# Optimization experiments

Hardware: AMD Instinct MI355X
Metric: run time of the kernel (lower is better)

The kernel has to match this reference:

```python
import jax, jax.numpy as jnp
import numpy as np

NUM_HEADS = 8

def conv1x1(w, x, b=None):
    # w: [O, C], x: [B, C, H, W] -> [B, O, H, W]
    y = jnp.einsum('oc,bchw->bohw', w, x)
    if b is not None:
        y = y + b[None, :, None, None]
    return y

def setup_inputs() -> dict:
    key = jax.random.key(0)
    ks = jax.random.split(key, 8)
    B, C, H, W = 8, 512, 32, 32
    s = lambda fan: 1.0 / np.sqrt(fan)
    return {
        'x': jax.random.normal(ks[0], (B, C, H, W), jnp.float32),
        'W_qkv': jax.random.normal(ks[1], (3 * C, C), jnp.float32) * s(C),
        'W_proj': jax.random.normal(ks[2], (C, C), jnp.float32) * s(C),
        'b_proj': jax.random.normal(ks[3], (C,), jnp.float32) * 0.01,
        'W_att1': jax.random.normal(ks[4], (C // 4, C), jnp.float32) * s(C),
        'b_att1': jax.random.normal(ks[5], (C // 4,), jnp.float32) * 0.01,
        'W_att2': jax.random.normal(ks[6], (1, C // 4), jnp.float32) * s(C // 4),
        'b_att2': jax.random.normal(ks[7], (1,), jnp.float32) * 0.01,
    }

def reference(x, W_qkv, W_proj, b_proj, W_att1, b_att1, W_att2, b_att2):
    B, C, H, W = x.shape
    nh = NUM_HEADS
    dh = C // nh
    N = H * W
    qkv = conv1x1(W_qkv, x)                      # [B, 3C, H, W]
    qkv = qkv.reshape(B, 3, nh, dh, N)
    qkv = jnp.transpose(qkv, (1, 0, 2, 4, 3))    # [3, B, nh, N, dh]
    q, k, v = qkv[0], qkv[1], qkv[2]
    attn = jnp.einsum('bhnd,bhmd->bhnm', q, k) * (dh ** -0.5)
    attn = jax.nn.softmax(attn, axis=-1)         # dropout is identity at eval
    o = jnp.einsum('bhnm,bhmd->bhnd', attn, v)   # [B, nh, N, dh]
    # Faithful to torch: transpose(1,2) then raw reshape to (B, C, H, W)
    o = jnp.swapaxes(o, 1, 2).reshape(B, C, H, W)
    out = conv1x1(W_proj, o, b_proj)             # [B, C, H, W]
    h1 = jax.nn.relu(conv1x1(W_att1, out, b_att1))
    spatial_att = jax.nn.sigmoid(conv1x1(W_att2, h1, b_att2))  # [B, 1, H, W]
    out = out * spatial_att
    return (out, spatial_att)
```

## Files before the change

kernel.cpp:

```cpp
#include <hip/hip_runtime.h>
#include <hip/hip_bf16.h>

using bf16 = __hip_bfloat16;
typedef __bf16 bf16x8 __attribute__((ext_vector_type(8)));
typedef float  f32x4  __attribute__((ext_vector_type(4)));


static constexpr int B  = 8;
static constexpr int C  = 512;
static constexpr int N  = 1024;
static constexpr int NH = 8;
static constexpr int DH = 64;
static constexpr int CQ = 128;

static constexpr float QSCALE = 0.125f * 1.44269504f;

static constexpr size_t QKV_OFF  = 0;
static constexpr size_t H1_OFF   = 25165824;

__device__ __forceinline__ unsigned pack2(float lo, float hi) {
  __hip_bfloat162 h = __float22bfloat162_rn(make_float2(lo, hi));
  return *(unsigned*)&h;
}
__device__ __forceinline__ int swz(int row, int col) {
  return row * 64 + ((((col >> 3) ^ row) & 7) << 3) + (col & 7);
}
__device__ __forceinline__ bf16x8 ldfrag(const short* tl, int row, int kk, int lane) {
  const int atom = 4 * kk + (lane >> 4);
  return *(const bf16x8*)&tl[row * 64 + (((atom ^ row) & 7) << 3)];
}
__device__ __forceinline__ bf16x8 ldfragF(const short* tl, int row, int kk, int lane) {
  const int atom = 4 * kk + (lane >> 4);
  return *(const bf16x8*)&tl[row * 64 + (((atom ^ row ^ (row >> 2)) & 7) << 3)];
}
__device__ __forceinline__ int fswz(int row, int col) {
  return row * 64 + ((((col >> 2) ^ row) & 15) << 2) + (col & 3);
}
__device__ __forceinline__ void swap32(unsigned &a, unsigned &b) {
  asm("v_permlane32_swap_b32 %0, %1" : "+v"(a), "+v"(b));
}
__device__ __forceinline__ void swap16(unsigned &a, unsigned &b) {
  asm("v_permlane16_swap_b32 %0, %1" : "+v"(a), "+v"(b));
}

__global__ __launch_bounds__(256, 3) void k_qkv(const float* __restrict__ W,
                                                const float* __restrict__ x,
                                                bf16* __restrict__ qkv) {
  __shared__ __align__(16) short Al[128 * 64];
  __shared__ __align__(16) short Bl[128 * 64];
  const int pt = blockIdx.x, ot = blockIdx.y, b = blockIdx.z;
  const int p0 = pt * 128, o0 = ot * 128;
  const int t = threadIdx.x, l = t & 63, w = t >> 6;
  const int wo = w & 1, wp = w >> 1;
  const int g = t >> 5, k32 = t & 31;
  const int r16 = t >> 4, q16 = t & 15;
  const float* xsrc = x + ((size_t)b * C + 8 * g) * N + p0 + 4 * k32;
  const float* wsrc = W + (size_t)(o0 + r16) * C + 4 * q16;
  unsigned upx[16], upw[16];
  auto ld = [&](int kc) {
    const float* xa = xsrc + (size_t)kc * N;
#pragma unroll
    for (int u = 0; u < 4; ++u) {
      float4 r0 = *(const float4*)(xa + (size_t)(2 * u) * N);
      float4 r1 = *(const float4*)(xa + (size_t)(2 * u + 1) * N);
      upx[4*u+0] = pack2(r0.x, r1.x);
      upx[4*u+1] = pack2(r0.y, r1.y);
      upx[4*u+2] = pack2(r0.z, r1.z);
      upx[4*u+3] = pack2(r0.w, r1.w);
    }
    const float* wa = wsrc + kc;
#pragma unroll
    for (int i = 0; i < 8; ++i) {
      float4 f = *(const float4*)(wa + (size_t)(16 * i) * C);
      upw[2*i]   = pack2(f.x, f.y);
      upw[2*i+1] = pack2(f.z, f.w);
    }
  };
  f32x4 acc[4][4] = {};
  ld(0);
  for (int kc = 0; kc < C; kc += 64) {
    __syncthreads();
#pragma unroll
    for (int j = 0; j < 4; ++j) {
      const int p = 4 * k32 + j;
      uint4 v = make_uint4(upx[j], upx[4 + j], upx[8 + j], upx[12 + j]);
      *(uint4*)&Al[p * 64 + (((g ^ p ^ (p >> 2)) & 7) << 3)] = v;
    }
#pragma unroll
    for (int i = 0; i < 8; ++i) {
      const int R = 16 * i + r16;
      *(uint2*)&Bl[R * 64 + ((((q16 >> 1) ^ R) & 7) << 3) + 4 * (q16 & 1)] =
          make_uint2(upw[2 * i], upw[2 * i + 1]);
    }
    __syncthreads();
    if (kc + 64 < C) ld(kc + 64);
#pragma unroll
    for (int kk = 0; kk < 2; ++kk) {
      bf16x8 af[4], bf[4];
#pragma unroll
      for (int i = 0; i < 4; ++i) af[i] = ldfrag(Bl, wo*64 + i*16 + (l&15), kk, l);
#pragma unroll
      for (int j = 0; j < 4; ++j) bf[j] = ldfragF(Al, wp*64 + j*16 + (l&15), kk, l);
#pragma unroll
      for (int i = 0; i < 4; ++i)
#pragma unroll
        for (int j = 0; j < 4; ++j)
          acc[i][j] = __builtin_amdgcn_mfma_f32_16x16x32_bf16(af[i], bf[j], acc[i][j], 0, 0, 0);
    }
  }
  const float qs = (ot < 4) ? QSCALE : 1.0f;
  __syncthreads();
  {
    short* T = wo ? Bl : Al;
#pragma unroll
    for (int i = 0; i < 4; ++i) {
      const int d = i * 16 + 4 * (l >> 4);
#pragma unroll
      for (int j = 0; j < 4; ++j) {
        const int p = wp * 64 + j * 16 + (l & 15);
        *(unsigned*)&T[swz(p, d)]     = pack2(acc[i][j][0] * qs, acc[i][j][1] * qs);
        *(unsigned*)&T[swz(p, d + 2)] = pack2(acc[i][j][2] * qs, acc[i][j][3] * qs);
      }
    }
  }
  __syncthreads();
  {
    const int oc0 = o0, oc1 = o0 + 64;
    bf16* dst0 = qkv + (size_t)(oc0 >> 9) * (B * NH * N * DH) +
                 (size_t)(b * NH + ((oc0 >> 6) & 7)) * N * DH + (size_t)p0 * DH;
    bf16* dst1 = qkv + (size_t)(oc1 >> 9) * (B * NH * N * DH) +
                 (size_t)(b * NH + ((oc1 >> 6) & 7)) * N * DH + (size_t)p0 * DH;
#pragma unroll
    for (int it = 0; it < 8; ++it) {
      const int e = t + 256 * it;
      const int tile = e >> 10, row = (e >> 3) & 127, atom = e & 7;
      const short* T = tile ? Bl : Al;
      uint4 val = *(const uint4*)&T[row * 64 + (((atom ^ row) & 7) << 3)];
      bf16* dst = tile ? dst1 : dst0;
      *(uint4*)(dst + (size_t)row * DH + atom * 8) = val;
    }
  }
}

__global__ __launch_bounds__(256) void k_attn(bf16* __restrict__ qkv) {
  __shared__ __align__(16) short Ql[64 * 64];
  __shared__ __align__(16) short Kl[64 * 64];
  __shared__ __align__(16) short Vt[64 * 64];
  const int bh = blockIdx.x, qt = blockIdx.y;
  const int t = threadIdx.x, l = t & 63, w = t >> 6;
  const bf16* kp = qkv + (size_t)B * NH * N * DH;
  const bf16* vp = kp + (size_t)B * NH * N * DH;
  const uint4* gkb = (const uint4*)(kp + (size_t)bh * N * DH);
  const uint4* gvb = (const uint4*)(vp + (size_t)bh * N * DH);
  const int kpr = t & 31, g = t >> 5;

  {
    const uint4* gq = (const uint4*)(qkv + ((size_t)bh * N + qt * 64) * DH);
    for (int c = t; c < 512; c += 256) {
      int row = c >> 3, atom = c & 7;
      *(uint4*)&Ql[row * 64 + (((atom ^ row) & 7) << 3)] = gq[c];
    }
  }
  __syncthreads();
  bf16x8 qf[2] = { ldfrag(Ql, w * 16 + (l & 15), 0, l),
                   ldfrag(Ql, w * 16 + (l & 15), 1, l) };
  f32x4 oacc[4] = {};
  f32x4 lacc = {};
  short* Pw = Ql + w * 1024;

  bf16x8 onesf;
#pragma unroll
  for (int i = 0; i < 8; ++i) onesf[i] = (__bf16)1.0f;

  uint4 kreg0, kreg1, v0, v1;
  auto ld = [&](int mt) {
    const uint4* gk = gkb + mt * 512;
    kreg0 = gk[t]; kreg1 = gk[t + 256];
    const uint4* gv = gvb + mt * 512;
    v0 = gv[16 * kpr + g]; v1 = gv[16 * kpr + 8 + g];
  };
  ld(0);

  for (int mt = 0; mt < 16; ++mt) {
    __syncthreads();
    {
      const int r0 = t >> 3, a0 = t & 7;
      *(uint4*)&Kl[r0 * 64 + (((a0 ^ r0) & 7) << 3)] = kreg0;
      const int r1 = r0 + 32;
      *(uint4*)&Kl[r1 * 64 + (((a0 ^ r1) & 7) << 3)] = kreg1;
      const unsigned* v0d = (const unsigned*)&v0;
      const unsigned* v1d = (const unsigned*)&v1;
#pragma unroll
      for (int j = 0; j < 8; ++j) {
        unsigned pk = __builtin_amdgcn_perm(v1d[j >> 1], v0d[j >> 1],
                                            (j & 1) ? 0x07060302u : 0x05040100u);
        *(unsigned*)&Vt[swz(g * 8 + j, 2 * kpr)] = pk;
      }
    }
    __syncthreads();
    if (mt < 15) ld(mt + 1);
    f32x4 sacc[4] = {};
#pragma unroll
    for (int kk = 0; kk < 2; ++kk)
#pragma unroll
      for (int kt = 0; kt < 4; ++kt) {
        bf16x8 af = ldfrag(Kl, kt * 16 + (l & 15), kk, l);
        sacc[kt] = __builtin_amdgcn_mfma_f32_16x16x32_bf16(af, qf[kk], sacc[kt], 0, 0, 0);
      }
    unsigned D[4][2];
#pragma unroll
    for (int kt = 0; kt < 4; ++kt) {
      float p0v = __builtin_exp2f(sacc[kt][0]);
      float p1v = __builtin_exp2f(sacc[kt][1]);
      float p2v = __builtin_exp2f(sacc[kt][2]);
      float p3v = __builtin_exp2f(sacc[kt][3]);
      D[kt][0] = pack2(p0v, p1v);
      D[kt][1] = pack2(p2v, p3v);
    }
#pragma unroll
    for (int kk = 0; kk < 2; ++kk) {
      unsigned a0 = D[2*kk][0], b0 = D[2*kk + 1][0];
      unsigned a1 = D[2*kk][1], b1 = D[2*kk + 1][1];
      swap32(a0, b0); swap16(a0, b0);
      swap32(a1, b1); swap16(a1, b1);
      uint4 pv = make_uint4(a0, a1, b0, b1);
      bf16x8 pbf = *(bf16x8*)&pv;
      lacc = __builtin_amdgcn_mfma_f32_16x16x32_bf16(onesf, pbf, lacc, 0, 0, 0);
#pragma unroll
      for (int dt = 0; dt < 4; ++dt) {
        bf16x8 av = ldfrag(Vt, dt * 16 + (l & 15), kk, l);
        oacc[dt] = __builtin_amdgcn_mfma_f32_16x16x32_bf16(av, pbf, oacc[dt], 0, 0, 0);
      }
    }
  }
  __syncthreads();
  const float inv = 1.f / lacc[0];
  const int qr = l & 15, cb0 = 4 * (l >> 4);
#pragma unroll
  for (int dt = 0; dt < 4; ++dt) {
    const int cb = dt * 16 + cb0;
    *(unsigned*)&Pw[swz(qr, cb)]     = pack2(oacc[dt][0] * inv, oacc[dt][1] * inv);
    *(unsigned*)&Pw[swz(qr, cb + 2)] = pack2(oacc[dt][2] * inv, oacc[dt][3] * inv);
  }
  __syncthreads();
  bf16* obase = qkv + ((size_t)bh * N + qt * 64 + w * 16) * DH;
#pragma unroll
  for (int i = 0; i < 2; ++i) {
    const int e = l + 64 * i, row = e >> 3, atom = e & 7;
    uint4 val = *(const uint4*)&Pw[row * 64 + (((atom ^ row) & 7) << 3)];
    *(uint4*)(obase + (size_t)row * DH + atom * 8) = val;
  }
}

__global__ __launch_bounds__(256) void k_proj(const float* __restrict__ Wp,
                                              const float* __restrict__ bp,
                                              const bf16* __restrict__ obuf,
                                              float* __restrict__ outd) {
  __shared__ __align__(16) short SM[8192];
  short* Wl = SM;
  short* Ot = SM + 4096;
  const int pt = blockIdx.x, ct = blockIdx.y, b = blockIdx.z;
  const int p0 = pt * 64, co0 = ct * 64;
  const int h = (p0 & 511) >> 6, eps = p0 >> 9;
  const int t = threadIdx.x, l = t & 63, w = t >> 6;
  const int r16 = t >> 4, q16 = t & 15;
  const int jp = t >> 3, a8 = t & 7;
  const float* wsrc = &Wp[(size_t)(co0 + r16) * C + 4 * q16];
  const bf16* obase = obuf + (size_t)(b * NH + h) * N * DH;
  float4 wreg[4]; uint4 or0, or1;
  auto ld = [&](int kc) {
    const float* wa = wsrc + kc;
#pragma unroll
    for (int i = 0; i < 4; ++i)
      wreg[i] = *(const float4*)(wa + (size_t)(16 * i) * C);
    const bf16* ob = obase + (size_t)(2 * (kc + 2 * jp) + eps) * 64 + 8 * a8;
    or0 = *(const uint4*)(ob);
    or1 = *(const uint4*)(ob + 128);
  };
  f32x4 acc[4] = {};
  ld(0);
  for (int kc = 0; kc < C; kc += 64) {
    __syncthreads();
#pragma unroll
    for (int i = 0; i < 4; ++i) {
      const int R = 16 * i + r16;
      *(uint2*)&Wl[R * 64 + ((((q16 >> 1) ^ R) & 7) << 3) + 4 * (q16 & 1)] =
          make_uint2(pack2(wreg[i].x, wreg[i].y), pack2(wreg[i].z, wreg[i].w));
    }
    {
      const unsigned* o0d = (const unsigned*)&or0;
      const unsigned* o1d = (const unsigned*)&or1;
#pragma unroll
      for (int dd = 0; dd < 8; ++dd) {
        unsigned pk = __builtin_amdgcn_perm(o1d[dd >> 1], o0d[dd >> 1],
                                            (dd & 1) ? 0x07060302u : 0x05040100u);
        const int row = 8 * a8 + dd;
        *(unsigned*)&Ot[row * 64 + ((((jp >> 2) ^ row ^ (row >> 2)) & 7) << 3) +
                        ((2 * jp) & 7)] = pk;
      }
    }
    __syncthreads();
    if (kc + 64 < C) ld(kc + 64);
    const int mrow = w * 16 + (l & 15);
#pragma unroll
    for (int kk = 0; kk < 2; ++kk) {
      bf16x8 a = ldfragF(Ot, mrow, kk, l);
#pragma unroll
      for (int nt = 0; nt < 4; ++nt) {
        bf16x8 bf = ldfrag(Wl, nt * 16 + (l & 15), kk, l);
        acc[nt] = __builtin_amdgcn_mfma_f32_16x16x32_bf16(a, bf, acc[nt], 0, 0, 0);
      }
    }
  }
  __syncthreads();
  {
    float* Ep = (float*)SM;
    const int pp = w * 16 + 4 * (l >> 4);
#pragma unroll
    for (int nt = 0; nt < 4; ++nt) {
      const int co = nt * 16 + (l & 15);
      const float bias = bp[co0 + co];
      *(float2*)&Ep[fswz(co, pp)]     = make_float2(acc[nt][0] + bias, acc[nt][1] + bias);
      *(float2*)&Ep[fswz(co, pp + 2)] = make_float2(acc[nt][2] + bias, acc[nt][3] + bias);
    }
  }
  __syncthreads();
  {
    const float* Ep = (const float*)SM;
#pragma unroll
    for (int it = 0; it < 4; ++it) {
      const int e = t + 256 * it;
      const int co = e >> 4, a = e & 15;
      float4 v = *(const float4*)&Ep[co * 64 + (((a ^ (co & 15)) & 15) << 2)];
      *(float4*)&outd[(size_t)b * C * N + (size_t)(co0 + co) * N + p0 + a * 4] = v;
    }
  }
}

__global__ __launch_bounds__(256) void k_att1(const float* __restrict__ W1,
                                              const float* __restrict__ b1,
                                              const float* __restrict__ outd,
                                              bf16* __restrict__ h1b) {
  __shared__ __align__(16) short Wl[64 * 64];
  __shared__ __align__(16) short Xt[64 * 64];
  const int pt = blockIdx.x, jt = blockIdx.y, b = blockIdx.z;
  const int p0 = pt * 64, j0 = jt * 64;
  const int t = threadIdx.x, l = t & 63, w = t >> 6;
  const int r16 = t >> 4, q16 = t & 15;
  const float* wsrc = &W1[(size_t)(j0 + r16) * C + 4 * q16];
  const float* xb = &outd[(size_t)b * C * N + p0 + 4 * q16];
  float4 wreg[4], xr[4];
  auto ld = [&](int kc) {
    const float* wa = wsrc + kc;
#pragma unroll
    for (int i = 0; i < 4; ++i)
      wreg[i] = *(const float4*)(wa + (size_t)(16 * i) * C);
#pragma unroll
    for (int i = 0; i < 4; ++i)
      xr[i] = *(const float4*)(xb + (size_t)(kc + 4 * r16 + i) * N);
  };
  f32x4 acc[4] = {};
  ld(0);
  for (int kc = 0; kc < C; kc += 64) {
    __syncthreads();
#pragma unroll
    for (int i = 0; i < 4; ++i) {
      const int R = 16 * i + r16;
      *(uint2*)&Wl[R * 64 + ((((q16 >> 1) ^ R) & 7) << 3) + 4 * (q16 & 1)] =
          make_uint2(pack2(wreg[i].x, wreg[i].y), pack2(wreg[i].z, wreg[i].w));
    }
    {
      const float* x0 = (const float*)&xr[0];
      const float* x1 = (const float*)&xr[1];
      const float* x2 = (const float*)&xr[2];
      const float* x3 = (const float*)&xr[3];
#pragma unroll
      for (int dd = 0; dd < 4; ++dd) {
        unsigned lo = pack2(x0[dd], x1[dd]);
        unsigned hi = pack2(x2[dd], x3[dd]);
        const int row = 4 * q16 + dd;
        *(uint2*)&Xt[row * 64 + ((((r16 >> 1) ^ row ^ (row >> 2)) & 7) << 3) +
                     ((4 * r16) & 7)] = make_uint2(lo, hi);
      }
    }
    __syncthreads();
    if (kc + 64 < C) ld(kc + 64);
    const int mrow = w * 16 + (l & 15);
#pragma unroll
    for (int kk = 0; kk < 2; ++kk) {
      bf16x8 a = ldfragF(Xt, mrow, kk, l);
#pragma unroll
      for (int nt = 0; nt < 4; ++nt) {
        bf16x8 bf = ldfrag(Wl, nt * 16 + (l & 15), kk, l);
        acc[nt] = __builtin_amdgcn_mfma_f32_16x16x32_bf16(a, bf, acc[nt], 0, 0, 0);
      }
    }
  }
  __syncthreads();
  {
    const int pp = w * 16 + 4 * (l >> 4);
#pragma unroll
    for (int nt = 0; nt < 4; ++nt) {
      const int jo = nt * 16 + (l & 15);
      const float bias = b1[j0 + jo];
      float v0 = fmaxf(acc[nt][0] + bias, 0.f), v1 = fmaxf(acc[nt][1] + bias, 0.f);
      float v2 = fmaxf(acc[nt][2] + bias, 0.f), v3 = fmaxf(acc[nt][3] + bias, 0.f);
      *(unsigned*)&Wl[swz(jo, pp)]     = pack2(v0, v1);
      *(unsigned*)&Wl[swz(jo, pp + 2)] = pack2(v2, v3);
    }
  }
  __syncthreads();
#pragma unroll
  for (int it = 0; it < 2; ++it) {
    const int e = t + 256 * it;
    const int row = e >> 3, atom = e & 7;
    uint4 val = *(const uint4*)&Wl[row * 64 + (((atom ^ row) & 7) << 3)];
    *(uint4*)((bf16*)h1b + (size_t)b * CQ * N + (size_t)(j0 + row) * N + p0 + atom * 8) = val;
  }
}

__global__ __launch_bounds__(256) void k_gate(const float* __restrict__ W2,
                                              const float* __restrict__ b2,
                                              const bf16* __restrict__ h1b,
                                              float* __restrict__ out0,
                                              float* __restrict__ out1) {
  __shared__ float red[8][32];
  __shared__ __align__(16) float att[32];
  const int blk = blockIdx.x, t = threadIdx.x;
  const int b = blk >> 5, p0 = (blk & 31) * 32;
  const int pl = t & 31, jg = t >> 5;
  float acc = 0.f;
  const bf16* hb = h1b + ((size_t)b * CQ + jg * 16) * N + p0 + pl;
#pragma unroll
  for (int jj = 0; jj < 16; ++jj)
    acc += W2[jg * 16 + jj] * __bfloat162float(hb[(size_t)jj * N]);
  red[jg][pl] = acc;
  __syncthreads();
  if (t < 32) {
    float a = b2[0];
#pragma unroll
    for (int k = 0; k < 8; ++k) a += red[k][t];
    const float sg = 1.f / (1.f + __expf(-a));
    att[t] = sg;
    out1[b * N + p0 + t] = sg;
  }
  __syncthreads();
  const int p4 = t & 7, cc = t >> 3;
  float4* ob4 = (float4*)(out0 + (size_t)b * C * N + p0);
  const float4 sg4 = *(const float4*)&att[4 * p4];
  for (int c = cc; c < C; c += 32) {
    float4 v = ob4[c * 256 + p4];
    v.x *= sg4.x; v.y *= sg4.y; v.z *= sg4.z; v.w *= sg4.w;
    ob4[c * 256 + p4] = v;
  }
}

extern "C" void kernel_launch(void* const* d_in, const int* in_sizes, int n_in,
                              void* d_out, int out_size, void* d_ws, size_t ws_size,
                              hipStream_t stream) {
  const float* x     = (const float*)d_in[0];
  const float* Wqkv  = (const float*)d_in[1];
  const float* Wproj = (const float*)d_in[2];
  const float* bproj = (const float*)d_in[3];
  const float* Watt1 = (const float*)d_in[4];
  const float* batt1 = (const float*)d_in[5];
  const float* Watt2 = (const float*)d_in[6];
  const float* batt2 = (const float*)d_in[7];

  char* ws = (char*)d_ws;
  bf16* qkvb = (bf16*)(ws + QKV_OFF);
  bf16* h1b  = (bf16*)(ws + H1_OFF);

  float* out0 = (float*)d_out;
  float* out1 = out0 + (size_t)B * C * N;

  k_qkv <<<dim3(8, 12, 8), 256, 0, stream>>>(Wqkv, x, qkvb);
  k_attn<<<dim3(64, 16),   256, 0, stream>>>(qkvb);
  k_proj<<<dim3(16, 8, 8), 256, 0, stream>>>(Wproj, bproj, qkvb, out0);
  k_att1<<<dim3(16, 2, 8), 256, 0, stream>>>(Watt1, batt1, out0, h1b);
  k_gate<<<256, 256, 0, stream>>>(Watt2, batt2, h1b, out0, out1);
}
```

Before: 171.7 us.

## Load K fragments directly from global into registers, drop K LDS staging

The attention kernel now reads K MFMA fragments straight from global memory into registers, double-buffered across two register sets, instead of staging K through shared memory. Only V is still transposed through LDS. The loop is unrolled by two to alternate the register buffers, and launch bounds now request 4 blocks per SM. This removes the LDS write and read traffic for K and shrinks shared memory per block, at the cost of more VGPRs and uncoalesced 16-byte global loads that rely on cache reuse across waves.

After: 212.7 us. +23.9%, slower.

```diff
diff --git a/kernel.cpp b/kernel.cpp
--- a/kernel.cpp
+++ b/kernel.cpp
@@ -142,15 +142,13 @@
   }
 }
 
-__global__ __launch_bounds__(256) void k_attn(bf16* __restrict__ qkv) {
+__global__ __launch_bounds__(256, 4) void k_attn(bf16* __restrict__ qkv) {
   __shared__ __align__(16) short Ql[64 * 64];
-  __shared__ __align__(16) short Kl[64 * 64];
   __shared__ __align__(16) short Vt[64 * 64];
   const int bh = blockIdx.x, qt = blockIdx.y;
   const int t = threadIdx.x, l = t & 63, w = t >> 6;
   const bf16* kp = qkv + (size_t)B * NH * N * DH;
   const bf16* vp = kp + (size_t)B * NH * N * DH;
-  const uint4* gkb = (const uint4*)(kp + (size_t)bh * N * DH);
   const uint4* gvb = (const uint4*)(vp + (size_t)bh * N * DH);
   const int kpr = t & 31, g = t >> 5;
 
@@ -161,6 +159,34 @@
       *(uint4*)&Ql[row * 64 + (((atom ^ row) & 7) << 3)] = gq[c];
     }
   }
+  const bf16* kfb = kp + (size_t)bh * N * DH + (size_t)(l & 15) * DH + (l >> 4) * 8;
+  bf16x8 kfA[8], kfB[8];
+  auto ldkf = [&](int mt, bf16x8* kf) {
+#pragma unroll
+    for (int kk = 0; kk < 2; ++kk)
+#pragma unroll
+      for (int kt = 0; kt < 4; ++kt)
+        kf[4 * kk + kt] =
+            *(const bf16x8*)(kfb + ((size_t)mt * 64 + kt * 16) * DH + kk * 32);
+  };
+  uint4 v0, v1;
+  auto ldv = [&](int mt) {
+    const uint4* gv = gvb + mt * 512;
+    v0 = gv[16 * kpr + g]; v1 = gv[16 * kpr + 8 + g];
+  };
+  auto stageV = [&]() {
+    const unsigned* v0d = (const unsigned*)&v0;
+    const unsigned* v1d = (const unsigned*)&v1;
+#pragma unroll
+    for (int j = 0; j < 8; ++j) {
+      unsigned pk = __builtin_amdgcn_perm(v1d[j >> 1], v0d[j >> 1],
+                                          (j & 1) ? 0x07060302u : 0x05040100u);
+      *(unsigned*)&Vt[swz(g * 8 + j, 2 * kpr)] = pk;
+    }
+  };
+
+  ldkf(0, kfA);
+  ldv(0);
   __syncthreads();
   bf16x8 qf[2] = { ldfrag(Ql, w * 16 + (l & 15), 0, l),
                    ldfrag(Ql, w * 16 + (l & 15), 1, l) };
@@ -172,41 +198,14 @@
 #pragma unroll
   for (int i = 0; i < 8; ++i) onesf[i] = (__bf16)1.0f;
 
-  uint4 kreg0, kreg1, v0, v1;
-  auto ld = [&](int mt) {
-    const uint4* gk = gkb + mt * 512;
-    kreg0 = gk[t]; kreg1 = gk[t + 256];
-    const uint4* gv = gvb + mt * 512;
-    v0 = gv[16 * kpr + g]; v1 = gv[16 * kpr + 8 + g];
-  };
-  ld(0);
-
-  for (int mt = 0; mt < 16; ++mt) {
-    __syncthreads();
-    {
-      const int r0 = t >> 3, a0 = t & 7;
-      *(uint4*)&Kl[r0 * 64 + (((a0 ^ r0) & 7) << 3)] = kreg0;
-      const int r1 = r0 + 32;
-      *(uint4*)&Kl[r1 * 64 + (((a0 ^ r1) & 7) << 3)] = kreg1;
-      const unsigned* v0d = (const unsigned*)&v0;
-      const unsigned* v1d = (const unsigned*)&v1;
-#pragma unroll
-      for (int j = 0; j < 8; ++j) {
-        unsigned pk = __builtin_amdgcn_perm(v1d[j >> 1], v0d[j >> 1],
-                                            (j & 1) ? 0x07060302u : 0x05040100u);
-        *(unsigned*)&Vt[swz(g * 8 + j, 2 * kpr)] = pk;
-      }
-    }
-    __syncthreads();
-    if (mt < 15) ld(mt + 1);
+  auto compute = [&](const bf16x8* kf) {
     f32x4 sacc[4] = {};
 #pragma unroll
     for (int kk = 0; kk < 2; ++kk)
 #pragma unroll
-      for (int kt = 0; kt < 4; ++kt) {
-        bf16x8 af = ldfrag(Kl, kt * 16 + (l & 15), kk, l);
-        sacc[kt] = __builtin_amdgcn_mfma_f32_16x16x32_bf16(af, qf[kk], sacc[kt], 0, 0, 0);
-      }
+      for (int kt = 0; kt < 4; ++kt)
+        sacc[kt] = __builtin_amdgcn_mfma_f32_16x16x32_bf16(kf[4*kk+kt], qf[kk],
+                                                           sacc[kt], 0, 0, 0);
     unsigned D[4][2];
 #pragma unroll
     for (int kt = 0; kt < 4; ++kt) {
@@ -232,6 +231,20 @@
         oacc[dt] = __builtin_amdgcn_mfma_f32_16x16x32_bf16(av, pbf, oacc[dt], 0, 0, 0);
       }
     }
+  };
+
+  for (int mt = 0; mt < 16; mt += 2) {
+    __syncthreads();
+    stageV();
+    __syncthreads();
+    ldv(mt + 1);
+    ldkf(mt + 1, kfB);
+    compute(kfA);
+    __syncthreads();
+    stageV();
+    __syncthreads();
+    if (mt < 14) { ldv(mt + 2); ldkf(mt + 2, kfA); }
+    compute(kfB);
   }
   __syncthreads();
   const float inv = 1.f / lacc[0];
```
